# Kernel optimization log

Hardware: AMD Instinct MI355X
Metric: run time of the kernel (lower is better)

## Reference

```python
import jax, jax.numpy as jnp
import numpy as np

B, T, X, E, H, L = 4096, 32, 256, 32, 512, 2  # batch, theta_size, x_size, n_masks, hidden, num_hidden_layers


def _prelu(v, a):
    # PReLU with per-channel slope a (broadcast [E,H] or [B,E,H] vs [B,E,H])
    return jnp.where(v >= 0, v, a * v)


def setup_inputs() -> dict:
    key = jax.random.key(0)
    ks = jax.random.split(key, 12)
    theta = jax.random.normal(ks[0], (B, T), dtype=jnp.float32)
    x = jax.random.normal(ks[1], (B, X), dtype=jnp.float32)
    masks = jax.random.randint(ks[2], (E, T), 0, 2, dtype=jnp.int32)
    masks = masks.at[:, 0].set(1)  # guarantee non-empty subsets
    D = T + X
    s_in = 1.0 / np.sqrt(D)
    s_h = 1.0 / np.sqrt(H)
    # first Linear, split into theta-part and x-part of the weight matrix
    W1t = jax.random.normal(ks[3], (E, T, H), dtype=jnp.float32) * s_in
    W1x = jax.random.normal(ks[4], (E, X, H), dtype=jnp.float32) * s_in
    b1 = jax.random.normal(ks[5], (E, H), dtype=jnp.float32) * s_in
    a1 = jnp.full((E, H), 0.25, dtype=jnp.float32)  # PReLU init
    # num_layers hidden Linear(H,H) + PReLU
    Wh = jax.random.normal(ks[6], (L, E, H, H), dtype=jnp.float32) * s_h
    bh = jax.random.normal(ks[7], (L, E, H), dtype=jnp.float32) * s_h
    ah = jnp.full((L, E, H), 0.25, dtype=jnp.float32)
    # output Linear(H, 1) -> squeeze(-1)
    Wo = jax.random.normal(ks[8], (E, H), dtype=jnp.float32) * s_h
    bo = jax.random.normal(ks[9], (E,), dtype=jnp.float32) * s_h
    return {"theta": theta, "x": x, "masks": masks, "W1t": W1t, "W1x": W1x,
            "b1": b1, "a1": a1, "Wh": Wh, "bh": bh, "ah": ah, "Wo": Wo, "bo": bo}


def reference(theta, x, masks, W1t, W1x, b1, a1, Wh, bh, ah, Wo, bo):
    # theta[..., mask] followed by Linear is equivalent to masking theta per
    # expert and contracting with the full per-expert theta weight block.
    m = masks.astype(theta.dtype)                      # [E, T]
    tm = theta[:, None, :] * m[None, :, :]             # [B, E, T]
    h = (jnp.einsum('bet,eth->beh', tm, W1t)
         + jnp.einsum('bx,exh->beh', x, W1x) + b1)     # [B, E, H]
    h = _prelu(h, a1)
    for i in range(Wh.shape[0]):                       # small fixed layer loop
        h = jnp.einsum('beh,ehk->bek', h, Wh[i]) + bh[i]
        h = _prelu(h, ah[i])
    # Linear(H,1).squeeze(-1), stacked over masks on the last dim -> [B, E]
    return jnp.einsum('beh,eh->be', h, Wo) + bo
```

## Files before the change

### kernel.cpp

```cpp
#include <hip/hip_runtime.h>
#include <stdint.h>

#define B_SZ 4096
#define T_SZ 32
#define X_SZ 256
#define E_SZ 32
#define H_SZ 512
#define BM   128

typedef __attribute__((ext_vector_type(8))) short  short8;
typedef __attribute__((ext_vector_type(4))) float  floatx4;

__device__ __forceinline__ unsigned pk2(float a, float b) {
  unsigned r;
  asm("v_cvt_pk_bf16_f32 %0, %1, %2" : "=v"(r) : "v"(a), "v"(b));
  return r;
}

__global__ __launch_bounds__(256) void prep_kernel(
    const float* __restrict__ W1t, const float* __restrict__ W1x,
    const int* __restrict__ masks, const float* __restrict__ Wh,
    uint4* __restrict__ wcat, uint4* __restrict__ whf) {
  __shared__ unsigned lds[16 * 516];
  const int c = blockIdx.x;
  const int t = threadIdx.x;

  const float* base;
  bool needMask = false;
  int e1 = 0;
  if (c >= 288) {
    int cc = c - 288;
    int le = cc >> 4, kt = cc & 15;
    base = Wh + ((size_t)le * H_SZ + kt * 32) * H_SZ;
  } else {
    int e = c / 9, kt = c - e * 9;
    e1 = e;
    if (kt == 0) { base = W1t + (size_t)e * T_SZ * H_SZ; needMask = true; }
    else          base = W1x + ((size_t)e * X_SZ + (kt - 1) * 32) * H_SZ;
  }

#pragma unroll
  for (int i = 0; i < 8; ++i) {
    int g  = i * 256 + t;
    int k2 = g >> 7, np = g & 127;
    const float* r0 = base + (size_t)(2 * k2) * H_SZ + np * 4;
    float4 a = *(const float4*)r0;
    float4 b = *(const float4*)(r0 + H_SZ);
    if (needMask) {
      float s0 = (float)masks[e1 * T_SZ + 2 * k2];
      float s1 = (float)masks[e1 * T_SZ + 2 * k2 + 1];
      a.x *= s0; a.y *= s0; a.z *= s0; a.w *= s0;
      b.x *= s1; b.y *= s1; b.z *= s1; b.w *= s1;
    }
    *(uint4*)&lds[k2 * 516 + np * 4] =
        make_uint4(pk2(a.x, b.x), pk2(a.y, b.y), pk2(a.z, b.z), pk2(a.w, b.w));
  }
  __syncthreads();

  uint4* outp = (c < 288) ? (wcat + (size_t)c * 2048)
                          : (whf + (size_t)(c - 288) * 2048);
  const int w = t >> 6, l = t & 63, q = l >> 4, l16 = l & 15;
#pragma unroll
  for (int j = 0; j < 8; ++j) {
    int nb = w * 8 + j;
    int n  = nb * 16 + l16;
    int kb = 4 * q;
    uint4 v;
    v.x = lds[(kb + 0) * 516 + n];
    v.y = lds[(kb + 1) * 516 + n];
    v.z = lds[(kb + 2) * 516 + n];
    v.w = lds[(kb + 3) * 516 + n];
    outp[nb * 64 + l] = v;
  }
}

__global__ __launch_bounds__(1024, 4) void mlp_kernel(
    const float* __restrict__ theta, const float* __restrict__ x,
    const short8* __restrict__ wcat, const short8* __restrict__ whf,
    const float* __restrict__ b1, const float* __restrict__ a1,
    const float* __restrict__ bh, const float* __restrict__ ah,
    const float* __restrict__ Wo, const float* __restrict__ bo,
    float* __restrict__ out) {
  __shared__ __align__(16) char smA[8 * 16 * 64 * 16];
  const int tid = threadIdx.x;
  const int bid = blockIdx.x;
  const int xcd = bid & 7;
  const int t8  = bid >> 3;
  const int e   = xcd * 4 + (t8 >> 5);
  const int m0  = (t8 & 31) * BM;
  const int w   = tid >> 6, l = tid & 63, l16 = l & 15, quad = l >> 4;
  const int rh  = w & 1;
  const int wc  = w >> 1;

  for (int g = tid; g < 9 * 512; g += 1024) {
    int lane = g & 63, mb = (g >> 6) & 7, kt = g >> 9;
    int row  = m0 + mb * 16 + (lane & 15);
    int ks   = (lane >> 4) * 8;
    const float* src = (kt == 0)
                           ? (theta + (size_t)row * T_SZ + ks)
                           : (x + (size_t)row * X_SZ + (kt - 1) * 32 + ks);
    float4 a = *(const float4*)src;
    float4 b = *(const float4*)(src + 4);
    *(uint4*)(smA + mb * 16384 + kt * 1024 + lane * 16) =
        make_uint4(pk2(a.x, a.y), pk2(a.z, a.w), pk2(b.x, b.y), pk2(b.z, b.w));
  }
  __syncthreads();

  floatx4 acc[4][4];
  const int u0 = wc * 256 + l;
  const char* dsb0 = smA + rh * 65536 + l * 16;

  auto gemm = [&](const short8* wbase, int nkt) {
#pragma unroll
    for (int m = 0; m < 4; ++m)
#pragma unroll
      for (int i = 0; i < 4; ++i) acc[m][i] = (floatx4)(0.f);
    short8 bA[4], bB[4];
    const short8* wu = wbase;
#pragma unroll
    for (int i = 0; i < 4; ++i) bA[i] = wu[u0 + i * 64];
    const char* dsb = dsb0;
    const int half = nkt >> 1;
#pragma unroll 1
    for (int j = 0; j < half; ++j) {
#pragma unroll
      for (int i = 0; i < 4; ++i) bB[i] = wu[2048 + u0 + i * 64];
      {
        short8 af[4];
#pragma unroll
        for (int m = 0; m < 4; ++m)
          af[m] = *(const short8*)(dsb + m * 16384);
#pragma unroll
        for (int m = 0; m < 4; ++m)
#pragma unroll
          for (int i = 0; i < 4; ++i)
            acc[m][i] = __builtin_amdgcn_mfma_f32_16x16x32_bf16(
                af[m], bA[i], acc[m][i], 0, 0, 0);
      }
      const short8* wn = (2 * j + 2 < nkt) ? wu + 4096 : wu;
#pragma unroll
      for (int i = 0; i < 4; ++i) bA[i] = wn[u0 + i * 64];
      {
        short8 af[4];
#pragma unroll
        for (int m = 0; m < 4; ++m)
          af[m] = *(const short8*)(dsb + m * 16384 + 1024);
#pragma unroll
        for (int m = 0; m < 4; ++m)
#pragma unroll
          for (int i = 0; i < 4; ++i)
            acc[m][i] = __builtin_amdgcn_mfma_f32_16x16x32_bf16(
                af[m], bB[i], acc[m][i], 0, 0, 0);
      }
      wu += 4096;
      dsb += 2048;
    }
    if (nkt & 1) {
      short8 af[4];
#pragma unroll
      for (int m = 0; m < 4; ++m)
        af[m] = *(const short8*)(dsb + m * 16384);
#pragma unroll
      for (int m = 0; m < 4; ++m)
#pragma unroll
        for (int i = 0; i < 4; ++i)
          acc[m][i] = __builtin_amdgcn_mfma_f32_16x16x32_bf16(
              af[m], bA[i], acc[m][i], 0, 0, 0);
    }
  };

  auto epi_store = [&](const float* bias, const float* slope) {
    float bb[4], aa[4];
#pragma unroll
    for (int i = 0; i < 4; ++i) {
      int col = wc * 64 + i * 16 + l16;
      bb[i] = bias[col];
      aa[i] = slope[col];
    }
    __syncthreads();
#pragma unroll
    for (int mb = 0; mb < 4; ++mb) {
#pragma unroll
      for (int i = 0; i < 4; ++i) {
        unsigned dw[4];
#pragma unroll
        for (int r = 0; r < 4; ++r) {
          float v = acc[mb][i][r] + bb[i];
          v = v >= 0.f ? v : aa[i] * v;
          float o  = __shfl_xor(v, 1, 64);
          float lo = (l16 & 1) ? o : v;
          float hi = (l16 & 1) ? v : o;
          dw[r] = pk2(lo, hi);
        }
        int rbase = (l16 & 1) * 2;
        int mbp   = rh * 4 + mb;
        int ktp   = wc * 2 + (i >> 1);
        int lhi   = ((i * 2 + (l16 >> 3)) & 3) * 16;
        char* ubase = smA + mbp * 16384 + ktp * 1024 + (l16 & 6) * 2;
#pragma unroll
        for (int rr = 0; rr < 2; ++rr) {
          int lane_p = (quad * 4 + rbase + rr) + lhi;
          *(unsigned*)(ubase + lane_p * 16) = dw[rbase + rr];
        }
      }
    }
    __syncthreads();
  };

  gemm(wcat + (size_t)e * 9 * 2048, 9);
  epi_store(b1 + (size_t)e * H_SZ, a1 + (size_t)e * H_SZ);
  gemm(whf + (size_t)e * 16 * 2048, 16);
  epi_store(bh + (size_t)e * H_SZ, ah + (size_t)e * H_SZ);
  gemm(whf + (size_t)(E_SZ + e) * 16 * 2048, 16);
  {
    float bb[4], aa[4], wo[4];
#pragma unroll
    for (int i = 0; i < 4; ++i) {
      int col = wc * 64 + i * 16 + l16;
      bb[i] = bh[(size_t)(E_SZ + e) * H_SZ + col];
      aa[i] = ah[(size_t)(E_SZ + e) * H_SZ + col];
      wo[i] = Wo[(size_t)e * H_SZ + col];
    }
    float ps[4][4];
#pragma unroll
    for (int m = 0; m < 4; ++m)
#pragma unroll
      for (int r = 0; r < 4; ++r) ps[m][r] = 0.f;
#pragma unroll
    for (int m = 0; m < 4; ++m)
#pragma unroll
      for (int i = 0; i < 4; ++i)
#pragma unroll
        for (int r = 0; r < 4; ++r) {
          float v = acc[m][i][r] + bb[i];
          v = v >= 0.f ? v : aa[i] * v;
          ps[m][r] += v * wo[i];
        }
#pragma unroll
    for (int d = 1; d < 16; d <<= 1)
#pragma unroll
      for (int m = 0; m < 4; ++m)
#pragma unroll
        for (int r = 0; r < 4; ++r) ps[m][r] += __shfl_xor(ps[m][r], d, 64);
    __syncthreads();
    float* scratch = (float*)smA;
    if (l16 == 0) {
#pragma unroll
      for (int m = 0; m < 4; ++m)
#pragma unroll
        for (int r = 0; r < 4; ++r)
          scratch[(rh * 64 + m * 16 + quad * 4 + r) * 8 + wc] = ps[m][r];
    }
    __syncthreads();
    if (tid < BM) {
      float s = 0.f;
#pragma unroll
      for (int ww = 0; ww < 8; ++ww) s += scratch[tid * 8 + ww];
      out[(size_t)(m0 + tid) * E_SZ + e] = s + bo[e];
    }
  }
}

extern "C" void kernel_launch(void* const* d_in, const int* in_sizes, int n_in,
                              void* d_out, int out_size, void* d_ws, size_t ws_size,
                              hipStream_t stream) {
  const float* theta = (const float*)d_in[0];
  const float* x     = (const float*)d_in[1];
  const int*   masks = (const int*)d_in[2];
  const float* W1t   = (const float*)d_in[3];
  const float* W1x   = (const float*)d_in[4];
  const float* b1    = (const float*)d_in[5];
  const float* a1    = (const float*)d_in[6];
  const float* Wh    = (const float*)d_in[7];
  const float* bh    = (const float*)d_in[8];
  const float* ah    = (const float*)d_in[9];
  const float* Wo    = (const float*)d_in[10];
  const float* bo    = (const float*)d_in[11];
  float* out = (float*)d_out;

  uint4* wcat = (uint4*)d_ws;
  uint4* whf  = (uint4*)((char*)d_ws + (size_t)E_SZ * 9 * 2048 * 16);

  prep_kernel<<<1312, 256, 0, stream>>>(W1t, W1x, masks, Wh, wcat, whf);
  mlp_kernel<<<1024, 1024, 0, stream>>>(theta, x, (const short8*)wcat,
                                        (const short8*)whf, b1, a1, bh, ah, Wo,
                                        bo, out);
}
```

Baseline: 327.3 us.

## Halve batch tile to 64 rows, use 512-thread blocks, add MFMA priority hints

Shrinks the per-block batch tile from 128 to 64 rows and the block from 16 to 8 waves, with each wave now covering all 64 rows for its column slice. The grid doubles to 2048 blocks and the block-to-expert mapping is changed so consecutive blocks spread across experts. MFMA sections are wrapped in s_setprio to raise issue priority. Smaller tiles halve LDS use and may raise occupancy and load balance, but each block re-reads the full weight matrix for half as many rows, so weight traffic per output row doubles.

```diff
diff --git a/kernel.cpp b/kernel.cpp
--- a/kernel.cpp
+++ b/kernel.cpp
@@ -6,7 +6,7 @@
 #define X_SZ 256
 #define E_SZ 32
 #define H_SZ 512
-#define BM   128
+#define BM   64
 
 typedef __attribute__((ext_vector_type(8))) short  short8;
 typedef __attribute__((ext_vector_type(4))) float  floatx4;
@@ -74,26 +74,23 @@
   }
 }
 
-__global__ __launch_bounds__(1024, 4) void mlp_kernel(
+__global__ __launch_bounds__(512, 4) void mlp_kernel(
     const float* __restrict__ theta, const float* __restrict__ x,
     const short8* __restrict__ wcat, const short8* __restrict__ whf,
     const float* __restrict__ b1, const float* __restrict__ a1,
     const float* __restrict__ bh, const float* __restrict__ ah,
     const float* __restrict__ Wo, const float* __restrict__ bo,
     float* __restrict__ out) {
-  __shared__ __align__(16) char smA[8 * 16 * 64 * 16];
+  __shared__ __align__(16) char smA[4 * 16 * 64 * 16];
   const int tid = threadIdx.x;
   const int bid = blockIdx.x;
-  const int xcd = bid & 7;
-  const int t8  = bid >> 3;
-  const int e   = xcd * 4 + (t8 >> 5);
-  const int m0  = (t8 & 31) * BM;
+  const int r5  = bid & 31;
+  const int e   = (r5 & 7) * 4 + (r5 >> 3);
+  const int m0  = (bid >> 5) * BM;
   const int w   = tid >> 6, l = tid & 63, l16 = l & 15, quad = l >> 4;
-  const int rh  = w & 1;
-  const int wc  = w >> 1;
-
-  for (int g = tid; g < 9 * 512; g += 1024) {
-    int lane = g & 63, mb = (g >> 6) & 7, kt = g >> 9;
+
+  for (int g = tid; g < 9 * 256; g += 512) {
+    int lane = g & 63, mb = (g >> 6) & 3, kt = g >> 8;
     int row  = m0 + mb * 16 + (lane & 15);
     int ks   = (lane >> 4) * 8;
     const float* src = (kt == 0)
@@ -107,8 +104,8 @@
   __syncthreads();
 
   floatx4 acc[4][4];
-  const int u0 = wc * 256 + l;
-  const char* dsb0 = smA + rh * 65536 + l * 16;
+  const int u0 = w * 256 + l;
+  const char* dsb0 = smA + l * 16;
 
   auto gemm = [&](const short8* wbase, int nkt) {
 #pragma unroll
@@ -123,34 +120,39 @@
     const int half = nkt >> 1;
 #pragma unroll 1
     for (int j = 0; j < half; ++j) {
-#pragma unroll
-      for (int i = 0; i < 4; ++i) bB[i] = wu[2048 + u0 + i * 64];
+      const short8* w1 = wu + 2048;
+#pragma unroll
+      for (int i = 0; i < 4; ++i) bB[i] = w1[u0 + i * 64];
       {
         short8 af[4];
 #pragma unroll
         for (int m = 0; m < 4; ++m)
           af[m] = *(const short8*)(dsb + m * 16384);
+        __builtin_amdgcn_s_setprio(1);
 #pragma unroll
         for (int m = 0; m < 4; ++m)
 #pragma unroll
           for (int i = 0; i < 4; ++i)
             acc[m][i] = __builtin_amdgcn_mfma_f32_16x16x32_bf16(
                 af[m], bA[i], acc[m][i], 0, 0, 0);
+        __builtin_amdgcn_s_setprio(0);
       }
-      const short8* wn = (2 * j + 2 < nkt) ? wu + 4096 : wu;
-#pragma unroll
-      for (int i = 0; i < 4; ++i) bA[i] = wn[u0 + i * 64];
+      const short8* w2 = (2 * j + 2 < nkt) ? wu + 4096 : wu;
+#pragma unroll
+      for (int i = 0; i < 4; ++i) bA[i] = w2[u0 + i * 64];
       {
         short8 af[4];
 #pragma unroll
         for (int m = 0; m < 4; ++m)
           af[m] = *(const short8*)(dsb + m * 16384 + 1024);
+        __builtin_amdgcn_s_setprio(1);
 #pragma unroll
         for (int m = 0; m < 4; ++m)
 #pragma unroll
           for (int i = 0; i < 4; ++i)
             acc[m][i] = __builtin_amdgcn_mfma_f32_16x16x32_bf16(
                 af[m], bB[i], acc[m][i], 0, 0, 0);
+        __builtin_amdgcn_s_setprio(0);
       }
       wu += 4096;
       dsb += 2048;
@@ -160,12 +162,14 @@
 #pragma unroll
       for (int m = 0; m < 4; ++m)
         af[m] = *(const short8*)(dsb + m * 16384);
+      __builtin_amdgcn_s_setprio(1);
 #pragma unroll
       for (int m = 0; m < 4; ++m)
 #pragma unroll
         for (int i = 0; i < 4; ++i)
           acc[m][i] = __builtin_amdgcn_mfma_f32_16x16x32_bf16(
               af[m], bA[i], acc[m][i], 0, 0, 0);
+      __builtin_amdgcn_s_setprio(0);
     }
   };
 
@@ -173,7 +177,7 @@
     float bb[4], aa[4];
 #pragma unroll
     for (int i = 0; i < 4; ++i) {
-      int col = wc * 64 + i * 16 + l16;
+      int col = w * 64 + i * 16 + l16;
       bb[i] = bias[col];
       aa[i] = slope[col];
     }
@@ -193,10 +197,9 @@
           dw[r] = pk2(lo, hi);
         }
         int rbase = (l16 & 1) * 2;
-        int mbp   = rh * 4 + mb;
-        int ktp   = wc * 2 + (i >> 1);
+        int ktp   = w * 2 + (i >> 1);
         int lhi   = ((i * 2 + (l16 >> 3)) & 3) * 16;
-        char* ubase = smA + mbp * 16384 + ktp * 1024 + (l16 & 6) * 2;
+        char* ubase = smA + mb * 16384 + ktp * 1024 + (l16 & 6) * 2;
 #pragma unroll
         for (int rr = 0; rr < 2; ++rr) {
           int lane_p = (quad * 4 + rbase + rr) + lhi;
@@ -216,7 +219,7 @@
     float bb[4], aa[4], wo[4];
 #pragma unroll
     for (int i = 0; i < 4; ++i) {
-      int col = wc * 64 + i * 16 + l16;
+      int col = w * 64 + i * 16 + l16;
       bb[i] = bh[(size_t)(E_SZ + e) * H_SZ + col];
       aa[i] = ah[(size_t)(E_SZ + e) * H_SZ + col];
       wo[i] = Wo[(size_t)e * H_SZ + col];
@@ -249,7 +252,7 @@
       for (int m = 0; m < 4; ++m)
 #pragma unroll
         for (int r = 0; r < 4; ++r)
-          scratch[(rh * 64 + m * 16 + quad * 4 + r) * 8 + wc] = ps[m][r];
+          scratch[(m * 16 + quad * 4 + r) * 8 + w] = ps[m][r];
     }
     __syncthreads();
     if (tid < BM) {
@@ -282,7 +285,7 @@
   uint4* whf  = (uint4*)((char*)d_ws + (size_t)E_SZ * 9 * 2048 * 16);
 
   prep_kernel<<<1312, 256, 0, stream>>>(W1t, W1x, masks, Wh, wcat, whf);
-  mlp_kernel<<<1024, 1024, 0, stream>>>(theta, x, (const short8*)wcat,
-                                        (const short8*)whf, b1, a1, bh, ah, Wo,
-                                        bo, out);
-}
+  mlp_kernel<<<2048, 512, 0, stream>>>(theta, x, (const short8*)wcat,
+                                       (const short8*)whf, b1, a1, bh, ah, Wo,
+                                       bo, out);
+}
```

Measured after the change: 307.2 us. 1.07x faster.
